# Performance work log

Measured on AMD Instinct MI355X. Metric: run time of the kernel, lower is better.

Reference implementation:

```python
import jax, jax.numpy as jnp
import numpy as np

DIM = 128
HEADS = 4
HEAD_DIM = DIM // HEADS
WS = (8, 8)
N = WS[0] * WS[1]
B = 4096
SCALE = HEAD_DIM ** -0.5


def _relative_position_index():
    # Swin-style relative position index, [N, N] int
    ch = np.arange(WS[0]); cw = np.arange(WS[1])
    coords = np.stack(np.meshgrid(ch, cw, indexing='ij'))          # [2, ws0, ws1]
    flat = coords.reshape(2, -1)                                    # [2, N]
    rel = flat[:, :, None] - flat[:, None, :]                       # [2, N, N]
    rel = rel.transpose(1, 2, 0)                                    # [N, N, 2]
    rel[:, :, 0] += WS[0] - 1
    rel[:, :, 1] += WS[1] - 1
    rel[:, :, 0] *= 2 * WS[1] - 1
    return jnp.asarray(rel.sum(-1))

REL_IDX = _relative_position_index()


def setup_inputs() -> dict:
    key = jax.random.key(0)
    ks = jax.random.split(key, 16)
    def lin(k, din, dout):
        return jax.random.normal(k, (din, dout), jnp.float32) * (din ** -0.5)
    return {
        'x': jax.random.normal(ks[0], (B, N, DIM), jnp.float32),
        'f': jax.random.normal(ks[1], (B, N, DIM), jnp.float32),
        'wq': lin(ks[2], DIM, DIM), 'bq': jnp.zeros((DIM,), jnp.float32),
        'wkv': lin(ks[3], DIM, 2 * DIM), 'bkv': jnp.zeros((2 * DIM,), jnp.float32),
        'wq_f': lin(ks[4], DIM, DIM), 'bq_f': jnp.zeros((DIM,), jnp.float32),
        'wkv_f': lin(ks[5], DIM, 2 * DIM), 'bkv_f': jnp.zeros((2 * DIM,), jnp.float32),
        'bias_table': jax.random.normal(ks[6], ((2 * WS[0] - 1) * (2 * WS[1] - 1), HEADS), jnp.float32) * 0.02,
        'wproj': lin(ks[7], DIM, DIM), 'bproj': jnp.zeros((DIM,), jnp.float32),
    }


def _qkv(t, wq, bq, wkv, bkv):
    Bn, Nn, C = t.shape
    q = (t @ wq + bq).reshape(Bn, Nn, HEADS, HEAD_DIM).transpose(0, 2, 1, 3)   # [B,H,N,D]
    kv = (t @ wkv + bkv).reshape(Bn, Nn, 2, HEADS, HEAD_DIM).transpose(2, 0, 3, 1, 4)
    return q, kv[0], kv[1]


def reference(x, f, wq, bq, wkv, bkv, wq_f, bq_f, wkv_f, bkv_f, bias_table, wproj, bproj):
    q, k, v = _qkv(x, wq, bq, wkv, bkv)
    attn = jnp.einsum('bhnd,bhmd->bhnm', q * SCALE, k)              # [B,H,N,N]
    q_f, k_f, _ = _qkv(f, wq_f, bq_f, wkv_f, bkv_f)
    attn_f = jnp.einsum('bhnd,bhmd->bhnm', q_f * SCALE, k_f)

    bias = bias_table[REL_IDX.reshape(-1)].reshape(N, N, HEADS)     # gather
    bias = bias.transpose(2, 0, 1)                                   # [H,N,N]
    ratio = attn.shape[-1] // bias.shape[-1]
    if ratio > 1:  # repeat last axis (no-op here since N == ws0*ws1)
        bias = jnp.repeat(bias, ratio, axis=-1)

    attn = (attn + bias[None]) * (attn_f + bias[None])               # joint modulation
    attn = jax.nn.softmax(attn, axis=-1)
    out = jnp.einsum('bhnm,bhmd->bhnd', attn, v)                     # [B,H,N,D]
    out = out.transpose(0, 2, 1, 3).reshape(x.shape[0], N, DIM)
    return out @ wproj + bproj
```

## Files before the change

kernel.cpp:

```cpp
#include <hip/hip_runtime.h>

typedef unsigned short u16;
typedef _Float16  f16x8  __attribute__((ext_vector_type(8)));
typedef _Float16  f16x4  __attribute__((ext_vector_type(4)));
typedef _Float16  f16x2  __attribute__((ext_vector_type(2)));
typedef float     f32x4  __attribute__((ext_vector_type(4)));

#define MFMA_F16(a,b,c)  __builtin_amdgcn_mfma_f32_16x16x32_f16(a,b,c,0,0,0)
#define PKRTZ(a,b) __builtin_bit_cast(f16x2, __builtin_amdgcn_cvt_pkrtz((a),(b)))

#define NTOK 64
#define DIM_ 128
#define SCALE_ 0.17677669529663687f

#define HREG 6784
#define KOFF 2304
#define VOFF 4608
#define SQK  36
#define SP   72
#define SAO  40
#define SVT  68
#define SMEM_U16 27136

__device__ __forceinline__ u16 f2h_u(float x) {
    _Float16 h = (_Float16)x;
    return __builtin_bit_cast(u16, h);
}

__global__ void wja_prep(const float* __restrict__ wq, const float* __restrict__ wkv,
                         const float* __restrict__ wq_f, const float* __restrict__ wkv_f,
                         const float* __restrict__ wproj, u16* __restrict__ ws)
{
    const int blk = blockIdx.x;
    const int l = threadIdx.x;
    const float* W; int ldw, colbase;
    if (blk < 32)       { W = wq;    ldw = 128; colbase = (blk      >> 2) * 16; }
    else if (blk < 96)  { W = wkv;   ldw = 256; colbase = ((blk- 32) >> 2) * 16; }
    else if (blk < 128) { W = wq_f;  ldw = 128; colbase = ((blk- 96) >> 2) * 16; }
    else if (blk < 160) { W = wkv_f; ldw = 256; colbase = ((blk-128) >> 2) * 16; }
    else                { W = wproj; ldw = 128; colbase = ((blk-160) >> 2) * 16; }
    const int ks = blk & 3;
    const int m = l & 15, g = l >> 4;
    u16* dst = ws + blk * 512 + l * 8;
    #pragma unroll
    for (int i = 0; i < 8; ++i)
        dst[i] = f2h_u(W[(size_t)(32*ks + 8*g + i) * ldw + colbase + m]);
}

__global__ __launch_bounds__(256, 2)
void wja_fused(
    const float* __restrict__ x, const float* __restrict__ f,
    const float* __restrict__ bq, const float* __restrict__ bkv,
    const float* __restrict__ bq_f, const float* __restrict__ bkv_f,
    const float* __restrict__ bproj, const float* __restrict__ btab,
    const u16* __restrict__ ws, float* __restrict__ out)
{
    __shared__ __align__(16) u16 smem[SMEM_U16];
    const int b    = blockIdx.x;
    const int tid  = threadIdx.x;
    const int w    = tid >> 6;
    const int lane = tid & 63;
    const int g    = lane >> 4;
    const int c    = lane & 15;
    const f32x4 zf4 = {0.f, 0.f, 0.f, 0.f};

    u16* const hb = smem + w * HREG;

    const float* const xb = x + (size_t)b * (NTOK * DIM_);
    const float* const fb = f + (size_t)b * (NTOK * DIM_);

    auto ldf16 = [](const float* p) -> f16x8 {
        f32x4 v0 = *(const f32x4*)p;
        f32x4 v1 = *(const f32x4*)(p + 4);
        struct Q { f16x2 a, b, c, d; } t;
        t.a = PKRTZ(v0[0], v0[1]);
        t.b = PKRTZ(v0[2], v0[3]);
        t.c = PKRTZ(v1[0], v1[1]);
        t.d = PKRTZ(v1[2], v1[3]);
        return __builtin_bit_cast(f16x8, t);
    };
    auto ldlds8 = [](const u16* p) -> f16x8 {
        struct P2 { f16x4 lo, hi; } t;
        t.lo = *(const f16x4*)p;
        t.hi = *(const f16x4*)(p + 4);
        return __builtin_bit_cast(f16x8, t);
    };

    f16x8 xfr[4], ffr[4];
    #pragma unroll
    for (int ks = 0; ks < 4; ++ks) {
        xfr[ks] = ldf16(xb + (16*w + c) * DIM_ + 32*ks + 8*g);
        ffr[ks] = ldf16(fb + (16*w + c) * DIM_ + 32*ks + 8*g);
    }

    auto gemmA = [&](const f16x8* afr, int wbase, const float* biasv, int which) {
        #pragma unroll
        for (int lct = 0; lct < 8; ++lct) {
            f32x4 acc = zf4;
            #pragma unroll
            for (int ks = 0; ks < 4; ++ks) {
                f16x8 bfr = *(const f16x8*)(ws + (wbase + 4*lct + ks) * 512 + lane * 8);
                acc = MFMA_F16(afr[ks], bfr, acc);
            }
            float bv = biasv[16*lct + c];
            const int hh = lct >> 1;
            const int cc = ((lct & 1) << 4) + c;
            if (which == 2) {
                struct H4 { f16x2 lo, hi; } t;
                t.lo = PKRTZ(acc[0] + bv, acc[1] + bv);
                t.hi = PKRTZ(acc[2] + bv, acc[3] + bv);
                *(f16x4*)(smem + hh*HREG + VOFF + cc*SVT + 16*w + 4*g) =
                    __builtin_bit_cast(f16x4, t);
            } else if (which == 1) {
                #pragma unroll
                for (int i = 0; i < 4; ++i)
                    smem[hh*HREG + KOFF + (16*w + 4*g + i)*SQK + cc] = f2h_u(acc[i] + bv);
            } else {
                #pragma unroll
                for (int i = 0; i < 4; ++i)
                    smem[hh*HREG + (16*w + 4*g + i)*SQK + cc] = f2h_u((acc[i] + bv) * SCALE_);
            }
        }
    };

    gemmA(xfr,   0, bq,        0);
    gemmA(xfr,  32, bkv,       1);
    gemmA(xfr,  64, bkv + 128, 2);
    __syncthreads();

    f32x4 S[4][4];
    {
        f16x8 qfr[4], kfr[4];
        #pragma unroll
        for (int t = 0; t < 4; ++t) {
            qfr[t] = ldlds8(hb + (16*t + c) * SQK + 8*g);
            kfr[t] = ldlds8(hb + KOFF + (16*t + c) * SQK + 8*g);
        }
        __builtin_amdgcn_s_setprio(1);
        #pragma unroll
        for (int mt = 0; mt < 4; ++mt)
            #pragma unroll
            for (int nt = 0; nt < 4; ++nt)
                S[mt][nt] = MFMA_F16(qfr[mt], kfr[nt], zf4);
        __builtin_amdgcn_s_setprio(0);
    }
    __syncthreads();

    gemmA(ffr,  96, bq_f,  0);
    gemmA(ffr, 128, bkv_f, 1);
    __syncthreads();

    {
        f16x8 kfr[4];
        #pragma unroll
        for (int t = 0; t < 4; ++t)
            kfr[t] = ldlds8(hb + KOFF + (16*t + c) * SQK + 8*g);
        #pragma unroll
        for (int mt = 0; mt < 4; ++mt) {
            f16x8 qfr = ldlds8(hb + (16*mt + c) * SQK + 8*g);
            __builtin_amdgcn_s_setprio(1);
            #pragma unroll
            for (int nt = 0; nt < 4; ++nt) {
                f32x4 sf = MFMA_F16(qfr, kfr[nt], zf4);
                int j = 16*nt + c;
                #pragma unroll
                for (int i = 0; i < 4; ++i) {
                    int r = 16*mt + 4*g + i;
                    int idx = ((r >> 3) - (j >> 3) + 7) * 15 + ((r & 7) - (j & 7) + 7);
                    float bv = btab[idx * 4 + w];
                    S[mt][nt][i] = (S[mt][nt][i] + bv) * (sf[i] + bv);
                }
            }
            __builtin_amdgcn_s_setprio(0);
        }
    }

    float rinv[4][4];
    #pragma unroll
    for (int mt = 0; mt < 4; ++mt)
        #pragma unroll
        for (int i = 0; i < 4; ++i) {
            float m = fmaxf(fmaxf(S[mt][0][i], S[mt][1][i]), fmaxf(S[mt][2][i], S[mt][3][i]));
            #pragma unroll
            for (int d = 1; d < 16; d <<= 1) m = fmaxf(m, __shfl_xor(m, d));
            float s0 = 0.f;
            #pragma unroll
            for (int nt = 0; nt < 4; ++nt) {
                float e = __expf(S[mt][nt][i] - m);
                S[mt][nt][i] = e;
                s0 += e;
            }
            #pragma unroll
            for (int d = 1; d < 16; d <<= 1) s0 += __shfl_xor(s0, d);
            rinv[mt][i] = 1.0f / s0;
        }

    #pragma unroll
    for (int mt = 0; mt < 4; ++mt)
        #pragma unroll
        for (int nt = 0; nt < 4; ++nt)
            #pragma unroll
            for (int i = 0; i < 4; ++i)
                hb[(16*mt + 4*g + i) * SP + 16*nt + c] = f2h_u(S[mt][nt][i] * rinv[mt][i]);

    f32x4 O[4][2] = { { zf4, zf4 }, { zf4, zf4 }, { zf4, zf4 }, { zf4, zf4 } };
    #pragma unroll
    for (int ks = 0; ks < 2; ++ks) {
        f16x8 pfr[4], vfr[2];
        #pragma unroll
        for (int mt = 0; mt < 4; ++mt)
            pfr[mt] = *(const f16x8*)(hb + (16*mt + c) * SP + 32*ks + 8*g);
        #pragma unroll
        for (int nt = 0; nt < 2; ++nt)
            vfr[nt] = ldlds8(hb + VOFF + (16*nt + c) * SVT + 32*ks + 8*g);
        __builtin_amdgcn_s_setprio(1);
        #pragma unroll
        for (int mt = 0; mt < 4; ++mt)
            #pragma unroll
            for (int nt = 0; nt < 2; ++nt)
                O[mt][nt] = MFMA_F16(pfr[mt], vfr[nt], O[mt][nt]);
        __builtin_amdgcn_s_setprio(0);
    }

    #pragma unroll
    for (int mt = 0; mt < 4; ++mt)
        #pragma unroll
        for (int nt = 0; nt < 2; ++nt)
            #pragma unroll
            for (int i = 0; i < 4; ++i)
                hb[(16*mt + 4*g + i) * SAO + 16*nt + c] = f2h_u(O[mt][nt][i]);

    __syncthreads();

    f32x4 PO[4][2] = { { zf4, zf4 }, { zf4, zf4 }, { zf4, zf4 }, { zf4, zf4 } };
    #pragma unroll
    for (int ks = 0; ks < 4; ++ks) {
        const u16* ao = smem + ks * HREG;
        f16x8 afr[4];
        #pragma unroll
        for (int mt = 0; mt < 4; ++mt)
            afr[mt] = *(const f16x8*)(ao + (16*mt + c) * SAO + 8*g);
        #pragma unroll
        for (int lct = 0; lct < 2; ++lct) {
            f16x8 bfr = *(const f16x8*)(ws + (160 + (2*w + lct) * 4 + ks) * 512 + lane * 8);
            #pragma unroll
            for (int mt = 0; mt < 4; ++mt)
                PO[mt][lct] = MFMA_F16(afr[mt], bfr, PO[mt][lct]);
        }
    }

    float* const ob = out + (size_t)b * 8192;
    #pragma unroll
    for (int lct = 0; lct < 2; ++lct) {
        float bv = bproj[32*w + 16*lct + c];
        #pragma unroll
        for (int mt = 0; mt < 4; ++mt)
            #pragma unroll
            for (int i = 0; i < 4; ++i)
                ob[(16*mt + 4*g + i) * 128 + 32*w + 16*lct + c] = PO[mt][lct][i] + bv;
    }
}

extern "C" void kernel_launch(void* const* d_in, const int* in_sizes, int n_in,
                              void* d_out, int out_size, void* d_ws, size_t ws_size,
                              hipStream_t stream)
{
    const float* x     = (const float*)d_in[0];
    const float* f     = (const float*)d_in[1];
    const float* wq    = (const float*)d_in[2];
    const float* bq    = (const float*)d_in[3];
    const float* wkv   = (const float*)d_in[4];
    const float* bkv   = (const float*)d_in[5];
    const float* wq_f  = (const float*)d_in[6];
    const float* bq_f  = (const float*)d_in[7];
    const float* wkv_f = (const float*)d_in[8];
    const float* bkv_f = (const float*)d_in[9];
    const float* btab  = (const float*)d_in[10];
    const float* wproj = (const float*)d_in[11];
    const float* bproj = (const float*)d_in[12];
    u16* ws    = (u16*)d_ws;
    float* out = (float*)d_out;

    hipLaunchKernelGGL(wja_prep, dim3(192), dim3(64), 0, stream,
                       wq, wkv, wq_f, wkv_f, wproj, ws);
    hipLaunchKernelGGL(wja_fused, dim3(4096), dim3(256), 0, stream,
                       x, f, bq, bkv, bq_f, bkv_f, bproj, btab, ws, out);
}
```

Measured before the change: 199.0 us.

## Precompute MFMA-layout bias tiles and fold bias into accumulator init

```diff
diff --git a/kernel.cpp b/kernel.cpp
--- a/kernel.cpp
+++ b/kernel.cpp
@@ -22,6 +22,8 @@
 #define SVT  68
 #define SMEM_U16 27136
 
+#define WS_TAB_F32 49152
+
 __device__ __forceinline__ u16 f2h_u(float x) {
     _Float16 h = (_Float16)x;
     return __builtin_bit_cast(u16, h);
@@ -29,22 +31,39 @@
 
 __global__ void wja_prep(const float* __restrict__ wq, const float* __restrict__ wkv,
                          const float* __restrict__ wq_f, const float* __restrict__ wkv_f,
-                         const float* __restrict__ wproj, u16* __restrict__ ws)
+                         const float* __restrict__ wproj, const float* __restrict__ btab,
+                         u16* __restrict__ ws)
 {
     const int blk = blockIdx.x;
     const int l = threadIdx.x;
-    const float* W; int ldw, colbase;
-    if (blk < 32)       { W = wq;    ldw = 128; colbase = (blk      >> 2) * 16; }
-    else if (blk < 96)  { W = wkv;   ldw = 256; colbase = ((blk- 32) >> 2) * 16; }
-    else if (blk < 128) { W = wq_f;  ldw = 128; colbase = ((blk- 96) >> 2) * 16; }
-    else if (blk < 160) { W = wkv_f; ldw = 256; colbase = ((blk-128) >> 2) * 16; }
-    else                { W = wproj; ldw = 128; colbase = ((blk-160) >> 2) * 16; }
-    const int ks = blk & 3;
-    const int m = l & 15, g = l >> 4;
-    u16* dst = ws + blk * 512 + l * 8;
-    #pragma unroll
-    for (int i = 0; i < 8; ++i)
-        dst[i] = f2h_u(W[(size_t)(32*ks + 8*g + i) * ldw + colbase + m]);
+    if (blk < 192) {
+        const float* W; int ldw, colbase;
+        if (blk < 32)       { W = wq;    ldw = 128; colbase = (blk      >> 2) * 16; }
+        else if (blk < 96)  { W = wkv;   ldw = 256; colbase = ((blk- 32) >> 2) * 16; }
+        else if (blk < 128) { W = wq_f;  ldw = 128; colbase = ((blk- 96) >> 2) * 16; }
+        else if (blk < 160) { W = wkv_f; ldw = 256; colbase = ((blk-128) >> 2) * 16; }
+        else                { W = wproj; ldw = 128; colbase = ((blk-160) >> 2) * 16; }
+        const int ks = blk & 3;
+        const int m = l & 15, g = l >> 4;
+        u16* dst = ws + blk * 512 + l * 8;
+        #pragma unroll
+        for (int i = 0; i < 8; ++i)
+            dst[i] = f2h_u(W[(size_t)(32*ks + 8*g + i) * ldw + colbase + m]);
+    } else {
+        const int h = blk - 192;
+        float* tab = (float*)ws + WS_TAB_F32 + h * 4096;
+        for (int e = l; e < 4096; e += 64) {
+            int i  = e & 3;
+            int cc = (e >> 2) & 15;
+            int g  = (e >> 6) & 3;
+            int nt = (e >> 8) & 3;
+            int mt = (e >> 10) & 3;
+            int r = 16*mt + 4*g + i;
+            int j = 16*nt + cc;
+            int idx = ((r >> 3) - (j >> 3) + 7) * 15 + ((r & 7) - (j & 7) + 7);
+            tab[e] = btab[idx * 4 + h];
+        }
+    }
 }
 
 __global__ __launch_bounds__(256, 2)
@@ -52,7 +71,7 @@
     const float* __restrict__ x, const float* __restrict__ f,
     const float* __restrict__ bq, const float* __restrict__ bkv,
     const float* __restrict__ bq_f, const float* __restrict__ bkv_f,
-    const float* __restrict__ bproj, const float* __restrict__ btab,
+    const float* __restrict__ bproj,
     const u16* __restrict__ ws, float* __restrict__ out)
 {
     __shared__ __align__(16) u16 smem[SMEM_U16];
@@ -65,6 +84,7 @@
     const f32x4 zf4 = {0.f, 0.f, 0.f, 0.f};
 
     u16* const hb = smem + w * HREG;
+    const float* const tabw = (const float*)ws + WS_TAB_F32 + w * 4096;
 
     const float* const xb = x + (size_t)b * (NTOK * DIM_);
     const float* const fb = f + (size_t)b * (NTOK * DIM_);
@@ -84,6 +104,9 @@
         t.lo = *(const f16x4*)p;
         t.hi = *(const f16x4*)(p + 4);
         return __builtin_bit_cast(f16x8, t);
+    };
+    auto btile = [&](int mt, int nt) -> f32x4 {
+        return *(const f32x4*)(tabw + ((mt*4 + nt)*4 + g)*64 + c*4);
     };
 
     f16x8 xfr[4], ffr[4];
@@ -136,13 +159,11 @@
             qfr[t] = ldlds8(hb + (16*t + c) * SQK + 8*g);
             kfr[t] = ldlds8(hb + KOFF + (16*t + c) * SQK + 8*g);
         }
-        __builtin_amdgcn_s_setprio(1);
         #pragma unroll
         for (int mt = 0; mt < 4; ++mt)
             #pragma unroll
             for (int nt = 0; nt < 4; ++nt)
-                S[mt][nt] = MFMA_F16(qfr[mt], kfr[nt], zf4);
-        __builtin_amdgcn_s_setprio(0);
+                S[mt][nt] = MFMA_F16(qfr[mt], kfr[nt], btile(mt, nt));
     }
     __syncthreads();
 
@@ -158,20 +179,13 @@
         #pragma unroll
         for (int mt = 0; mt < 4; ++mt) {
             f16x8 qfr = ldlds8(hb + (16*mt + c) * SQK + 8*g);
-            __builtin_amdgcn_s_setprio(1);
             #pragma unroll
             for (int nt = 0; nt < 4; ++nt) {
-                f32x4 sf = MFMA_F16(qfr, kfr[nt], zf4);
-                int j = 16*nt + c;
+                f32x4 sf = MFMA_F16(qfr, kfr[nt], btile(mt, nt));
                 #pragma unroll
-                for (int i = 0; i < 4; ++i) {
-                    int r = 16*mt + 4*g + i;
-                    int idx = ((r >> 3) - (j >> 3) + 7) * 15 + ((r & 7) - (j & 7) + 7);
-                    float bv = btab[idx * 4 + w];
-                    S[mt][nt][i] = (S[mt][nt][i] + bv) * (sf[i] + bv);
-                }
+                for (int i = 0; i < 4; ++i)
+                    S[mt][nt][i] *= sf[i];
             }
-            __builtin_amdgcn_s_setprio(0);
         }
     }
 
@@ -192,7 +206,7 @@
             }
             #pragma unroll
             for (int d = 1; d < 16; d <<= 1) s0 += __shfl_xor(s0, d);
-            rinv[mt][i] = 1.0f / s0;
+            rinv[mt][i] = __builtin_amdgcn_rcpf(s0);
         }
 
     #pragma unroll
@@ -201,7 +215,7 @@
         for (int nt = 0; nt < 4; ++nt)
             #pragma unroll
             for (int i = 0; i < 4; ++i)
-                hb[(16*mt + 4*g + i) * SP + 16*nt + c] = f2h_u(S[mt][nt][i] * rinv[mt][i]);
+                hb[(16*mt + 4*g + i) * SP + 16*nt + c] = f2h_u(S[mt][nt][i]);
 
     f32x4 O[4][2] = { { zf4, zf4 }, { zf4, zf4 }, { zf4, zf4 }, { zf4, zf4 } };
     #pragma unroll
@@ -213,13 +227,11 @@
         #pragma unroll
         for (int nt = 0; nt < 2; ++nt)
             vfr[nt] = ldlds8(hb + VOFF + (16*nt + c) * SVT + 32*ks + 8*g);
-        __builtin_amdgcn_s_setprio(1);
         #pragma unroll
         for (int mt = 0; mt < 4; ++mt)
             #pragma unroll
             for (int nt = 0; nt < 2; ++nt)
                 O[mt][nt] = MFMA_F16(pfr[mt], vfr[nt], O[mt][nt]);
-        __builtin_amdgcn_s_setprio(0);
     }
 
     #pragma unroll
@@ -228,7 +240,7 @@
         for (int nt = 0; nt < 2; ++nt)
             #pragma unroll
             for (int i = 0; i < 4; ++i)
-                hb[(16*mt + 4*g + i) * SAO + 16*nt + c] = f2h_u(O[mt][nt][i]);
+                hb[(16*mt + 4*g + i) * SAO + 16*nt + c] = f2h_u(O[mt][nt][i] * rinv[mt][i]);
 
     __syncthreads();
 
@@ -281,8 +293,8 @@
     u16* ws    = (u16*)d_ws;
     float* out = (float*)d_out;
 
-    hipLaunchKernelGGL(wja_prep, dim3(192), dim3(64), 0, stream,
-                       wq, wkv, wq_f, wkv_f, wproj, ws);
+    hipLaunchKernelGGL(wja_prep, dim3(196), dim3(64), 0, stream,
+                       wq, wkv, wq_f, wkv_f, wproj, btab, ws);
     hipLaunchKernelGGL(wja_fused, dim3(4096), dim3(256), 0, stream,
-                       x, f, bq, bkv, bq_f, bkv_f, bproj, btab, ws, out);
+                       x, f, bq, bkv, bq_f, bkv_f, bproj, ws, out);
 }
```

Result: faster. 185.2 us, median of 2 (-6.9%).
